# Optimization experiments

Measured on AMD Instinct MI355X. Metric: run time of the kernel, lower is better.

The kernel has to match this reference:

```python
import jax, jax.numpy as jnp
import numpy as np

GROUPS = 32
EPS = 1e-5


def group_norm(x, gamma, beta):
    # x: [B, C, H, W]; normalize over (C//G, H, W) within each of G groups
    B, C, H, W = x.shape
    xg = x.reshape(B, GROUPS, C // GROUPS, H, W)
    mean = xg.mean(axis=(2, 3, 4), keepdims=True)
    var = xg.var(axis=(2, 3, 4), keepdims=True)
    xg = (xg - mean) * jax.lax.rsqrt(var + EPS)
    x = xg.reshape(B, C, H, W)
    return x * gamma[None, :, None, None] + beta[None, :, None, None]


def conv1x1(x, W, b):
    # 1x1 conv == pointwise linear over channels. x: [B,C,H,W], W: [Cout,Cin]
    return jnp.einsum('oc,bchw->bohw', W, x) + b[None, :, None, None]


def setup_inputs() -> dict:
    key = jax.random.key(0)
    ks = jax.random.split(key, 6)
    B, C, H, W = 16, 512, 32, 32
    scale = 1.0 / np.sqrt(C)  # ~kaiming-ish init for 1x1 convs
    return {
        'x': jax.random.normal(ks[0], (B, C, H, W), jnp.float32),
        'gn_gamma': jnp.ones((C,), jnp.float32),
        'gn_beta': jnp.zeros((C,), jnp.float32),
        'Wq': jax.random.normal(ks[1], (C, C), jnp.float32) * scale,
        'bq': jnp.zeros((C,), jnp.float32),
        'Wk': jax.random.normal(ks[2], (C, C), jnp.float32) * scale,
        'bk': jnp.zeros((C,), jnp.float32),
        'Wv': jax.random.normal(ks[3], (C, C), jnp.float32) * scale,
        'bv': jnp.zeros((C,), jnp.float32),
        'Wp': jax.random.normal(ks[4], (C, C), jnp.float32) * scale,
        'bp': jnp.zeros((C,), jnp.float32),
    }


def reference(x, gn_gamma, gn_beta, Wq, bq, Wk, bk, Wv, bv, Wp, bp):
    B, C, H, W = x.shape
    h = group_norm(x, gn_gamma, gn_beta)
    q = conv1x1(h, Wq, bq).reshape(B, C, H * W)  # [B,C,T]
    k = conv1x1(h, Wk, bk).reshape(B, C, H * W)
    v = conv1x1(h, Wv, bv).reshape(B, C, H * W)
    # scores [B, T(query), S(key)] = q^T k, scaled by C^{-1/2}
    w = jnp.einsum('bct,bcs->bts', q, k) * (C ** -0.5)
    w = jax.nn.softmax(w, axis=-1)
    h = jnp.einsum('bts,bcs->bct', w, v).reshape(B, C, H, W)
    h = conv1x1(h, Wp, bp)
    return x + h
```

## Files before the change

### kernel.cpp

```cpp
#include <hip/hip_runtime.h>

typedef unsigned short u16;
typedef __bf16 bf16x8 __attribute__((ext_vector_type(8)));
typedef float f32x16 __attribute__((ext_vector_type(16)));

__device__ __forceinline__ u16 f2bf(float f) {
    unsigned u = __builtin_bit_cast(unsigned, f);
    u += 0x7fffu + ((u >> 16) & 1u);
    return (u16)(u >> 16);
}
__device__ __forceinline__ float bf2f(u16 h) {
    return __builtin_bit_cast(float, (unsigned)h << 16);
}

#define GLDS16(g, l) __builtin_amdgcn_global_load_lds( \
    (const __attribute__((address_space(1))) void*)(g), \
    (__attribute__((address_space(3))) void*)(l), 16, 0, 0)

#define QK_SCALE 0.044194173824159216f

__global__ __launch_bounds__(256) void convert_kernel(
    const float* __restrict__ Wq, const float* __restrict__ Wk,
    const float* __restrict__ Wv, const float* __restrict__ Wp,
    const float* __restrict__ bq, const float* __restrict__ bk,
    const float* __restrict__ bv,
    u16* __restrict__ Wqkv, u16* __restrict__ Wpb, float* __restrict__ bqkv)
{
    int idx = blockIdx.x * 256 + threadIdx.x;
    if (idx < 786432) {
        int which = idx >> 18;
        int off   = idx & 262143;
        if (which == 0)
            Wqkv[idx] = f2bf(Wq[off] * QK_SCALE);
        else
            Wqkv[idx] = f2bf(((which == 1) ? Wk : Wv)[off]);
    } else {
        int off = idx - 786432;
        Wpb[off] = f2bf(Wp[off]);
    }
    if (idx < 1536) {
        float bvv = (idx < 512) ? bq[idx] * QK_SCALE
                  : (idx < 1024) ? bk[idx & 511] : bv[idx & 511];
        bqkv[idx] = bvv;
    }
}

__global__ __launch_bounds__(256) void gn_stats(
    const float* __restrict__ x, float2* __restrict__ stats)
{
    const int g = blockIdx.x, b = blockIdx.y, tid = threadIdx.x;
    const float* xg = x + ((size_t)b * 512 + (size_t)g * 16) * 1024;

    float s = 0.f, s2 = 0.f;
    const float4* x4 = (const float4*)xg;
    #pragma unroll 4
    for (int i = tid; i < 4096; i += 256) {
        float4 v = x4[i];
        s  += v.x + v.y + v.z + v.w;
        s2 += v.x * v.x + v.y * v.y + v.z * v.z + v.w * v.w;
    }
    #pragma unroll
    for (int off = 32; off; off >>= 1) {
        s  += __shfl_down(s, off);
        s2 += __shfl_down(s2, off);
    }
    __shared__ float rs[4], rs2[4];
    const int w = tid >> 6;
    if ((tid & 63) == 0) { rs[w] = s; rs2[w] = s2; }
    __syncthreads();
    if (tid == 0) {
        float S  = rs[0] + rs[1] + rs[2] + rs[3];
        float S2 = rs2[0] + rs2[1] + rs2[2] + rs2[3];
        float mean = S * (1.f / 16384.f);
        float var  = S2 * (1.f / 16384.f) - mean * mean;
        stats[b * 32 + g] = make_float2(mean, rsqrtf(var + 1e-5f));
    }
}

__global__ __launch_bounds__(256) void gn_apply(
    const float* __restrict__ x, const float* __restrict__ gamma,
    const float* __restrict__ beta, const float2* __restrict__ stats,
    u16* __restrict__ ht)
{
    const int tc = blockIdx.x, b = blockIdx.y, tid = threadIdx.x;
    const int t0 = tc * 32;

    __shared__ float2 st[32];
    __shared__ float ga[512], be[512];
    __shared__ __align__(16) u16 tile[512 * 32];

    if (tid < 32) st[tid] = stats[b * 32 + tid];
    for (int c = tid; c < 512; c += 256) { ga[c] = gamma[c]; be[c] = beta[c]; }
    __syncthreads();

    #pragma unroll
    for (int pass = 0; pass < 16; pass++) {
        const int c = pass * 32 + (tid >> 3);
        const int f = tid & 7;
        float4 v = *(const float4*)(x + ((size_t)(b * 512 + c)) * 1024 + t0 + f * 4);
        float2 s = st[c >> 4];
        float sc = s.y * ga[c];
        float sh = be[c] - s.x * sc;
        ushort4 hv = {f2bf(v.x * sc + sh), f2bf(v.y * sc + sh),
                      f2bf(v.z * sc + sh), f2bf(v.w * sc + sh)};
        const int slot = f ^ (c & 7) ^ ((c >> 3) & 7);
        *(ushort4*)(tile + c * 32 + slot * 4) = hv;
    }
    __syncthreads();

    #pragma unroll
    for (int p = 0; p < 8; p++) {
        const int t = p * 4 + (tid >> 6);
        const int l = tid & 63;
        u16 tmp[8];
        #pragma unroll
        for (int e = 0; e < 8; e++) {
            const int c = l * 8 + e;
            const int slot = (t >> 2) ^ (c & 7) ^ ((c >> 3) & 7);
            tmp[e] = tile[c * 32 + slot * 4 + (t & 3)];
        }
        *(uint4*)(ht + ((size_t)b * 1024 + t0 + t) * 512 + l * 8) = *(uint4*)tmp;
    }
}

__global__ __launch_bounds__(256) void softmax_kernel(u16* __restrict__ scores)
{
    const int row  = blockIdx.x * 4 + (threadIdx.x >> 6);
    const int lane = threadIdx.x & 63;
    u16* p = scores + (size_t)row * 1024 + lane * 16;

    uint4 w0 = ((const uint4*)p)[0];
    uint4 w1 = ((const uint4*)p)[1];
    unsigned wd[8] = {w0.x, w0.y, w0.z, w0.w, w1.x, w1.y, w1.z, w1.w};
    float v[16];
    #pragma unroll
    for (int i = 0; i < 8; i++) {
        v[2 * i]     = __builtin_bit_cast(float, wd[i] << 16);
        v[2 * i + 1] = __builtin_bit_cast(float, wd[i] & 0xffff0000u);
    }
    float m = v[0];
    #pragma unroll
    for (int i = 1; i < 16; i++) m = fmaxf(m, v[i]);
    #pragma unroll
    for (int off = 1; off < 64; off <<= 1) m = fmaxf(m, __shfl_xor(m, off));

    float s = 0.f;
    #pragma unroll
    for (int i = 0; i < 16; i++) { v[i] = __expf(v[i] - m); s += v[i]; }
    #pragma unroll
    for (int off = 1; off < 64; off <<= 1) s += __shfl_xor(s, off);
    const float inv = 1.0f / s;

    #pragma unroll
    for (int i = 0; i < 8; i++) {
        unsigned lo = f2bf(v[2 * i] * inv);
        unsigned hi = f2bf(v[2 * i + 1] * inv);
        wd[i] = lo | (hi << 16);
    }
    ((uint4*)p)[0] = make_uint4(wd[0], wd[1], wd[2], wd[3]);
    ((uint4*)p)[1] = make_uint4(wd[4], wd[5], wd[6], wd[7]);
}

template <int MODE>
__global__ __launch_bounds__(256, 4) void gemm_nt(
    const u16* __restrict__ A, const u16* __restrict__ B,
    size_t strideA, size_t strideB, int lda, int ldb, int K,
    u16* __restrict__ o0, u16* __restrict__ o1, u16* __restrict__ o2,
    float* __restrict__ fo, const float* __restrict__ bias,
    const float* __restrict__ xres)
{
    __shared__ __align__(16) u16 sm[16384];
    u16* As = sm;
    u16* Bs = sm + 8192;

    const int tid   = threadIdx.x;
    const int lane  = tid & 63;
    const int wave  = tid >> 6;
    const int wm    = (wave >> 1) * 64;
    const int wn    = (wave & 1) * 64;
    const int l31   = lane & 31;
    const int khalf = lane >> 5;

    const int gx = gridDim.x, gy = gridDim.y;
    int f = blockIdx.x + gx * (blockIdx.y + gy * blockIdx.z);
    const int nwg = gx * gy * (int)gridDim.z;
    f = (f & 7) * (nwg >> 3) + (f >> 3);
    const int bx  = f % gx;
    const int byz = f / gx;
    const int by  = byz % gy;
    const int b   = byz / gy;

    const u16* Ab = A + (size_t)b * strideA + (size_t)by * 128 * lda;
    const u16* Bb = B + (size_t)b * strideB + (size_t)bx * 128 * ldb;

    const int srow = lane >> 3;
    const int sc   = lane & 7;
    const int scg  = sc ^ srow;

    f32x16 acc[2][2] = {};

    for (int k0 = 0; k0 < K; k0 += 64) {
        __syncthreads();
        #pragma unroll
        for (int s = 0; s < 4; s++) {
            const int r = wave * 32 + s * 8 + srow;
            GLDS16(Ab + (size_t)r * lda + k0 + scg * 8, As + r * 64 + sc * 8);
            GLDS16(Bb + (size_t)r * ldb + k0 + scg * 8, Bs + r * 64 + sc * 8);
        }
        __syncthreads();

        #pragma unroll
        for (int ks = 0; ks < 4; ks++) {
            const int cidx = ks * 2 + khalf;
            const int slot = (cidx ^ (lane & 7)) * 8;
            bf16x8 af[2], bfr[2];
            #pragma unroll
            for (int i = 0; i < 2; i++)
                af[i] = *(const bf16x8*)(As + (wm + i * 32 + l31) * 64 + slot);
            #pragma unroll
            for (int j = 0; j < 2; j++)
                bfr[j] = *(const bf16x8*)(Bs + (wn + j * 32 + l31) * 64 + slot);
            #pragma unroll
            for (int i = 0; i < 2; i++)
                #pragma unroll
                for (int j = 0; j < 2; j++)
                    acc[i][j] = __builtin_amdgcn_mfma_f32_32x32x16_bf16(
                        af[i], bfr[j], acc[i][j], 0, 0, 0);
        }
    }

    const int N0 = bx * 128;
    const int M0 = by * 128;

    if (MODE == 0 && N0 < 1024) {
        const int m_base = M0 + wm + 4 * khalf;
        const int n_base = N0 + wn + l31;
        #pragma unroll
        for (int i = 0; i < 2; i++) {
            #pragma unroll
            for (int j = 0; j < 2; j++) {
                const int n  = n_base + j * 32;
                const float bv = bias[n];
                u16* dst = (n < 512) ? o0 : o1;
                const int nn = n & 511;
                #pragma unroll
                for (int g = 0; g < 4; g++) {
                    const int m = m_base + i * 32 + 8 * g;
                    dst[((size_t)b * 1024 + m) * 512 + nn]     = f2bf(acc[i][j][4 * g]     + bv);
                    dst[((size_t)b * 1024 + m + 1) * 512 + nn] = f2bf(acc[i][j][4 * g + 1] + bv);
                    dst[((size_t)b * 1024 + m + 2) * 512 + nn] = f2bf(acc[i][j][4 * g + 2] + bv);
                    dst[((size_t)b * 1024 + m + 3) * 512 + nn] = f2bf(acc[i][j][4 * g + 3] + bv);
                }
            }
        }
    } else if (MODE != 3) {
        __syncthreads();
        #pragma unroll
        for (int i = 0; i < 2; i++) {
            #pragma unroll
            for (int j = 0; j < 2; j++) {
                const int n = wn + j * 32 + l31;
                const float bv = (MODE == 0) ? bias[N0 + n] : 0.f;
                #pragma unroll
                for (int g = 0; g < 4; g++) {
                    const int m = wm + 4 * khalf + i * 32 + 8 * g;
                    ushort4 hv = {f2bf(acc[i][j][4 * g]     + bv),
                                  f2bf(acc[i][j][4 * g + 1] + bv),
                                  f2bf(acc[i][j][4 * g + 2] + bv),
                                  f2bf(acc[i][j][4 * g + 3] + bv)};
                    *(ushort4*)(sm + n * 128 + (((m >> 3) ^ (n & 15)) << 3) + (m & 7)) = hv;
                }
            }
        }
        __syncthreads();
        #pragma unroll
        for (int p = 0; p < 8; p++) {
            const int n  = p * 16 + (tid >> 4);
            const int gi = tid & 15;
            uint4 v = *(const uint4*)(sm + n * 128 + ((gi ^ (n & 15)) << 3));
            u16* dst;
            if (MODE == 0)      dst = o2 + ((size_t)b * 512 + (N0 - 1024 + n)) * 1024 + M0;
            else if (MODE == 1) dst = o0 + ((size_t)b * 1024 + N0 + n) * 1024 + M0;
            else                dst = o0 + ((size_t)b * 1024 + N0 + n) * 512 + M0;
            *(uint4*)(dst + gi * 8) = v;
        }
    } else {
        float* smf = (float*)sm;
        #pragma unroll
        for (int i = 0; i < 2; i++) {
            __syncthreads();
            #pragma unroll
            for (int j = 0; j < 2; j++) {
                const int n = wn + j * 32 + l31;
                #pragma unroll
                for (int g = 0; g < 4; g++) {
                    const int mIdx = 4 * khalf + 8 * g + ((wm >> 6) << 5);
                    float4 v4 = {acc[i][j][4 * g],     acc[i][j][4 * g + 1],
                                 acc[i][j][4 * g + 2], acc[i][j][4 * g + 3]};
                    *(float4*)(smf + n * 64 + (((mIdx >> 2) ^ (n & 15)) << 2)) = v4;
                }
            }
            __syncthreads();
            #pragma unroll
            for (int p = 0; p < 8; p++) {
                const int n  = p * 16 + (tid >> 4);
                const int gi = tid & 15;
                float4 v = *(const float4*)(smf + n * 64 + ((gi ^ (n & 15)) << 2));
                const int m = (gi & 7) * 4 + ((gi >> 3) << 6) + 32 * i;
                const size_t off = ((size_t)b * 512 + N0 + n) * 1024 + M0 + m;
                const float bv = bias[N0 + n];
                const float4 xv = *(const float4*)(xres + off);
                float4 ov = {v.x + bv + xv.x, v.y + bv + xv.y,
                             v.z + bv + xv.z, v.w + bv + xv.w};
                *(float4*)(fo + off) = ov;
            }
        }
    }
}

extern "C" void kernel_launch(void* const* d_in, const int* in_sizes, int n_in,
                              void* d_out, int out_size, void* d_ws, size_t ws_size,
                              hipStream_t stream)
{
    const float* x     = (const float*)d_in[0];
    const float* gamma = (const float*)d_in[1];
    const float* beta  = (const float*)d_in[2];
    const float* Wq    = (const float*)d_in[3];
    const float* bq    = (const float*)d_in[4];
    const float* Wk    = (const float*)d_in[5];
    const float* bk    = (const float*)d_in[6];
    const float* Wv    = (const float*)d_in[7];
    const float* bv    = (const float*)d_in[8];
    const float* Wp    = (const float*)d_in[9];
    const float* bp    = (const float*)d_in[10];

    char* ws = (char*)d_ws;
    u16*   Wqkv   = (u16*)(ws + 0);
    u16*   Wpb    = (u16*)(ws + 1572864);
    float* bqkv   = (float*)(ws + 2097152);
    u16*   ht     = (u16*)(ws + 2105344);
    u16*   kt     = (u16*)(ws + 18882560);
    u16*   vv     = (u16*)(ws + 35659776);
    u16*   scores = (u16*)(ws + 52436992);
    u16*   qt  = (u16*)d_out;
    float2* stats = (float2*)((char*)d_out + 16777216);
    u16*   h2  = ht;
    float* out = (float*)d_out;

    convert_kernel<<<4096, 256, 0, stream>>>(Wq, Wk, Wv, Wp, bq, bk, bv,
                                             Wqkv, Wpb, bqkv);
    gn_stats<<<dim3(32, 16), 256, 0, stream>>>(x, stats);
    gn_apply<<<dim3(32, 16), 256, 0, stream>>>(x, gamma, beta, stats, ht);

    gemm_nt<0><<<dim3(12, 8, 16), 256, 0, stream>>>(
        ht, Wqkv, 524288, 0, 512, 512, 512,
        qt, kt, vv, nullptr, bqkv, nullptr);

    gemm_nt<1><<<dim3(8, 8, 16), 256, 0, stream>>>(
        kt, qt, 524288, 524288, 512, 512, 512,
        scores, nullptr, nullptr, nullptr, nullptr, nullptr);

    softmax_kernel<<<4096, 256, 0, stream>>>(scores);

    gemm_nt<2><<<dim3(8, 4, 16), 256, 0, stream>>>(
        vv, scores, 524288, 1048576, 1024, 1024, 1024,
        h2, nullptr, nullptr, nullptr, nullptr, nullptr);

    gemm_nt<3><<<dim3(4, 8, 16), 256, 0, stream>>>(
        h2, Wpb, 524288, 0, 512, 512, 512,
        nullptr, nullptr, nullptr, out, bp, x);
}
```

Before: 232.2 us.

## Replace GEMM with 256x128 tile, 512-thread, triple-buffered async pipeline

Rewrites the shared GEMM kernel to use 256x128 output tiles with 8 waves and 16x16x32 MFMAs. Global-to-LDS loads are triple-buffered and issued two K-steps ahead with partial vmcnt waits, replacing the synchronous load-then-compute loop. Epilogues are restaged through LDS for coalesced writes, including the Q/K row-major path. It uses much more LDS (144KB) and halves the grid sizes, which lowers occupancy and the number of workgroups.

```diff
diff --git a/kernel.cpp b/kernel.cpp
--- a/kernel.cpp
+++ b/kernel.cpp
@@ -2,15 +2,12 @@
 
 typedef unsigned short u16;
 typedef __bf16 bf16x8 __attribute__((ext_vector_type(8)));
-typedef float f32x16 __attribute__((ext_vector_type(16)));
+typedef float f32x4 __attribute__((ext_vector_type(4)));
 
 __device__ __forceinline__ u16 f2bf(float f) {
     unsigned u = __builtin_bit_cast(unsigned, f);
     u += 0x7fffu + ((u >> 16) & 1u);
     return (u16)(u >> 16);
-}
-__device__ __forceinline__ float bf2f(u16 h) {
-    return __builtin_bit_cast(float, (unsigned)h << 16);
 }
 
 #define GLDS16(g, l) __builtin_amdgcn_global_load_lds( \
@@ -162,24 +159,22 @@
 }
 
 template <int MODE>
-__global__ __launch_bounds__(256, 4) void gemm_nt(
+__global__ __launch_bounds__(512, 2) void gemm_big(
     const u16* __restrict__ A, const u16* __restrict__ B,
     size_t strideA, size_t strideB, int lda, int ldb, int K,
     u16* __restrict__ o0, u16* __restrict__ o1, u16* __restrict__ o2,
     float* __restrict__ fo, const float* __restrict__ bias,
     const float* __restrict__ xres)
 {
-    __shared__ __align__(16) u16 sm[16384];
-    u16* As = sm;
-    u16* Bs = sm + 8192;
-
-    const int tid   = threadIdx.x;
-    const int lane  = tid & 63;
-    const int wave  = tid >> 6;
-    const int wm    = (wave >> 1) * 64;
-    const int wn    = (wave & 1) * 64;
-    const int l31   = lane & 31;
-    const int khalf = lane >> 5;
+    __shared__ __align__(16) u16 smem[73728];
+    u16* As = smem;
+    u16* Bs = smem + 49152;
+
+    const int tid  = threadIdx.x;
+    const int lane = tid & 63;
+    const int wave = tid >> 6;
+    const int wm   = (wave & 3) * 64;
+    const int wn   = (wave >> 2) * 64;
 
     const int gx = gridDim.x, gy = gridDim.y;
     int f = blockIdx.x + gx * (blockIdx.y + gy * blockIdx.z);
@@ -190,130 +185,168 @@
     const int by  = byz % gy;
     const int b   = byz / gy;
 
-    const u16* Ab = A + (size_t)b * strideA + (size_t)by * 128 * lda;
+    const u16* Ab = A + (size_t)b * strideA + (size_t)by * 256 * lda;
     const u16* Bb = B + (size_t)b * strideB + (size_t)bx * 128 * ldb;
 
-    const int srow = lane >> 3;
-    const int sc   = lane & 7;
-    const int scg  = sc ^ srow;
-
-    f32x16 acc[2][2] = {};
-
-    for (int k0 = 0; k0 < K; k0 += 64) {
+    const int srow = tid >> 3;
+    const int sc   = tid & 7;
+    const int scg  = sc ^ (srow & 7);
+
+    const u16* aSrc[4]; int aDst[4];
+    #pragma unroll
+    for (int u = 0; u < 4; u++) {
+        aSrc[u] = Ab + (size_t)(u * 64 + srow) * lda + scg * 8;
+        aDst[u] = (u * 64 + srow) * 64 + sc * 8;
+    }
+    const u16* bSrc[2]; int bDst[2];
+    #pragma unroll
+    for (int u = 0; u < 2; u++) {
+        bSrc[u] = Bb + (size_t)(u * 64 + srow) * ldb + scg * 8;
+        bDst[u] = (u * 64 + srow) * 64 + sc * 8;
+    }
+
+#define STAGEBIG(ko, sb) do { \
+    _Pragma("unroll") \
+    for (int u = 0; u < 4; u++) \
+        GLDS16(aSrc[u] + (ko), As + (sb) * 16384 + aDst[u]); \
+    _Pragma("unroll") \
+    for (int u = 0; u < 2; u++) \
+        GLDS16(bSrc[u] + (ko), Bs + (sb) * 8192 + bDst[u]); \
+} while (0)
+
+    const int l15 = lane & 15, lh = lane >> 4, rx = lane & 7;
+    int aOff[4][2], bOff[4][2];
+    #pragma unroll
+    for (int i = 0; i < 4; i++)
+        #pragma unroll
+        for (int ks = 0; ks < 2; ks++) {
+            const int slot = ((ks << 2) + lh) ^ rx;
+            aOff[i][ks] = (wm + i * 16 + l15) * 64 + slot * 8;
+            bOff[i][ks] = (wn + i * 16 + l15) * 64 + slot * 8;
+        }
+
+    f32x4 acc[4][4] = {};
+    const int NT = K >> 6;
+
+    STAGEBIG(0, 0);
+    STAGEBIG(64, 1);
+
+    int cbuf = 0, sbuf = 2;
+    for (int t = 0; t < NT; ++t) {
+        if (t == NT - 1) asm volatile("s_waitcnt vmcnt(0)" ::: "memory");
+        else             asm volatile("s_waitcnt vmcnt(6)" ::: "memory");
+        __builtin_amdgcn_s_barrier();
+        __builtin_amdgcn_sched_barrier(0);
+
+        if (t + 2 < NT) STAGEBIG((t + 2) * 64, sbuf);
+        __builtin_amdgcn_sched_barrier(0);
+
+        const u16* Ac = As + cbuf * 16384;
+        const u16* Bc = Bs + cbuf * 8192;
+        bf16x8 af[4][2], bf[4][2];
+        #pragma unroll
+        for (int i = 0; i < 4; i++)
+            #pragma unroll
+            for (int ks = 0; ks < 2; ks++) {
+                af[i][ks] = *(const bf16x8*)(Ac + aOff[i][ks]);
+                bf[i][ks] = *(const bf16x8*)(Bc + bOff[i][ks]);
+            }
+
+        __builtin_amdgcn_s_setprio(1);
+        #pragma unroll
+        for (int ks = 0; ks < 2; ks++)
+            #pragma unroll
+            for (int mi = 0; mi < 4; mi++)
+                #pragma unroll
+                for (int nj = 0; nj < 4; nj++)
+                    acc[mi][nj] = __builtin_amdgcn_mfma_f32_16x16x32_bf16(
+                        af[mi][ks], bf[nj][ks], acc[mi][nj], 0, 0, 0);
+        __builtin_amdgcn_s_setprio(0);
+
+        cbuf = (cbuf == 2) ? 0 : cbuf + 1;
+        sbuf = (sbuf == 2) ? 0 : sbuf + 1;
+    }
+#undef STAGEBIG
+
+    const int N0 = bx * 128;
+    const int M0 = by * 256;
+
+    __syncthreads();
+
+    if (MODE != 3) {
+        #pragma unroll
+        for (int mi = 0; mi < 4; mi++) {
+            const int mq = wm + mi * 16 + lh * 4;
+            #pragma unroll
+            for (int nj = 0; nj < 4; nj++) {
+                const int n = wn + nj * 16 + l15;
+                float bv = 0.f;
+                if (MODE == 0) bv = bias[N0 + n];
+                ushort4 hv = {f2bf(acc[mi][nj][0] + bv), f2bf(acc[mi][nj][1] + bv),
+                              f2bf(acc[mi][nj][2] + bv), f2bf(acc[mi][nj][3] + bv)};
+                *(ushort4*)((char*)smem + n * 512 +
+                            ((((mq >> 3) ^ (n & 31))) << 4) + ((mq >> 2) & 1) * 8) = hv;
+            }
+        }
         __syncthreads();
-        #pragma unroll
-        for (int s = 0; s < 4; s++) {
-            const int r = wave * 32 + s * 8 + srow;
-            GLDS16(Ab + (size_t)r * lda + k0 + scg * 8, As + r * 64 + sc * 8);
-            GLDS16(Bb + (size_t)r * ldb + k0 + scg * 8, Bs + r * 64 + sc * 8);
+
+        if (MODE == 0 && N0 < 1024) {
+            #pragma unroll
+            for (int p = 0; p < 8; p++) {
+                const int m  = p * 32 + (tid >> 4);
+                const int ci = tid & 15;
+                u16 tmp[8];
+                #pragma unroll
+                for (int e = 0; e < 8; e++) {
+                    const int n = ci * 8 + e;
+                    tmp[e] = *(const u16*)((char*)smem + n * 512 +
+                             (((m >> 3) ^ (n & 31)) << 4) + (m & 7) * 2);
+                }
+                u16* dst = (N0 < 512) ? o0 : o1;
+                const int nn = (N0 & 511) + ci * 8;
+                *(uint4*)(dst + ((size_t)b * 1024 + M0 + m) * 512 + nn) = *(uint4*)tmp;
+            }
+        } else {
+            #pragma unroll
+            for (int p = 0; p < 8; p++) {
+                const int n  = p * 16 + (tid >> 5);
+                const int gi = tid & 31;
+                uint4 v4 = *(const uint4*)((char*)smem + n * 512 +
+                                           ((gi ^ (n & 31)) << 4));
+                u16* dst;
+                if (MODE == 0)      dst = o2 + ((size_t)b * 512 + (N0 - 1024) + n) * 1024 + M0;
+                else if (MODE == 1) dst = o0 + ((size_t)b * 1024 + N0 + n) * 1024 + M0;
+                else                dst = o0 + ((size_t)b * 1024 + N0 + n) * 512 + M0;
+                *(uint4*)(dst + gi * 8) = v4;
+            }
+        }
+    } else {
+        float* smf = (float*)smem;
+        #pragma unroll
+        for (int mi = 0; mi < 4; mi++) {
+            const int mq = wm + mi * 16 + lh * 4;
+            #pragma unroll
+            for (int nj = 0; nj < 4; nj++) {
+                const int n = wn + nj * 16 + l15;
+                float4 v4 = {acc[mi][nj][0], acc[mi][nj][1],
+                             acc[mi][nj][2], acc[mi][nj][3]};
+                *(float4*)((char*)smf + n * 1024 +
+                           (((mq >> 2) ^ (n & 63)) << 4)) = v4;
+            }
         }
         __syncthreads();
-
-        #pragma unroll
-        for (int ks = 0; ks < 4; ks++) {
-            const int cidx = ks * 2 + khalf;
-            const int slot = (cidx ^ (lane & 7)) * 8;
-            bf16x8 af[2], bfr[2];
-            #pragma unroll
-            for (int i = 0; i < 2; i++)
-                af[i] = *(const bf16x8*)(As + (wm + i * 32 + l31) * 64 + slot);
-            #pragma unroll
-            for (int j = 0; j < 2; j++)
-                bfr[j] = *(const bf16x8*)(Bs + (wn + j * 32 + l31) * 64 + slot);
-            #pragma unroll
-            for (int i = 0; i < 2; i++)
-                #pragma unroll
-                for (int j = 0; j < 2; j++)
-                    acc[i][j] = __builtin_amdgcn_mfma_f32_32x32x16_bf16(
-                        af[i], bfr[j], acc[i][j], 0, 0, 0);
-        }
-    }
-
-    const int N0 = bx * 128;
-    const int M0 = by * 128;
-
-    if (MODE == 0 && N0 < 1024) {
-        const int m_base = M0 + wm + 4 * khalf;
-        const int n_base = N0 + wn + l31;
-        #pragma unroll
-        for (int i = 0; i < 2; i++) {
-            #pragma unroll
-            for (int j = 0; j < 2; j++) {
-                const int n  = n_base + j * 32;
-                const float bv = bias[n];
-                u16* dst = (n < 512) ? o0 : o1;
-                const int nn = n & 511;
-                #pragma unroll
-                for (int g = 0; g < 4; g++) {
-                    const int m = m_base + i * 32 + 8 * g;
-                    dst[((size_t)b * 1024 + m) * 512 + nn]     = f2bf(acc[i][j][4 * g]     + bv);
-                    dst[((size_t)b * 1024 + m + 1) * 512 + nn] = f2bf(acc[i][j][4 * g + 1] + bv);
-                    dst[((size_t)b * 1024 + m + 2) * 512 + nn] = f2bf(acc[i][j][4 * g + 2] + bv);
-                    dst[((size_t)b * 1024 + m + 3) * 512 + nn] = f2bf(acc[i][j][4 * g + 3] + bv);
-                }
-            }
-        }
-    } else if (MODE != 3) {
-        __syncthreads();
-        #pragma unroll
-        for (int i = 0; i < 2; i++) {
-            #pragma unroll
-            for (int j = 0; j < 2; j++) {
-                const int n = wn + j * 32 + l31;
-                const float bv = (MODE == 0) ? bias[N0 + n] : 0.f;
-                #pragma unroll
-                for (int g = 0; g < 4; g++) {
-                    const int m = wm + 4 * khalf + i * 32 + 8 * g;
-                    ushort4 hv = {f2bf(acc[i][j][4 * g]     + bv),
-                                  f2bf(acc[i][j][4 * g + 1] + bv),
-                                  f2bf(acc[i][j][4 * g + 2] + bv),
-                                  f2bf(acc[i][j][4 * g + 3] + bv)};
-                    *(ushort4*)(sm + n * 128 + (((m >> 3) ^ (n & 15)) << 3) + (m & 7)) = hv;
-                }
-            }
-        }
-        __syncthreads();
-        #pragma unroll
-        for (int p = 0; p < 8; p++) {
-            const int n  = p * 16 + (tid >> 4);
-            const int gi = tid & 15;
-            uint4 v = *(const uint4*)(sm + n * 128 + ((gi ^ (n & 15)) << 3));
-            u16* dst;
-            if (MODE == 0)      dst = o2 + ((size_t)b * 512 + (N0 - 1024 + n)) * 1024 + M0;
-            else if (MODE == 1) dst = o0 + ((size_t)b * 1024 + N0 + n) * 1024 + M0;
-            else                dst = o0 + ((size_t)b * 1024 + N0 + n) * 512 + M0;
-            *(uint4*)(dst + gi * 8) = v;
-        }
-    } else {
-        float* smf = (float*)sm;
-        #pragma unroll
-        for (int i = 0; i < 2; i++) {
-            __syncthreads();
-            #pragma unroll
-            for (int j = 0; j < 2; j++) {
-                const int n = wn + j * 32 + l31;
-                #pragma unroll
-                for (int g = 0; g < 4; g++) {
-                    const int mIdx = 4 * khalf + 8 * g + ((wm >> 6) << 5);
-                    float4 v4 = {acc[i][j][4 * g],     acc[i][j][4 * g + 1],
-                                 acc[i][j][4 * g + 2], acc[i][j][4 * g + 3]};
-                    *(float4*)(smf + n * 64 + (((mIdx >> 2) ^ (n & 15)) << 2)) = v4;
-                }
-            }
-            __syncthreads();
-            #pragma unroll
-            for (int p = 0; p < 8; p++) {
-                const int n  = p * 16 + (tid >> 4);
-                const int gi = tid & 15;
-                float4 v = *(const float4*)(smf + n * 64 + ((gi ^ (n & 15)) << 2));
-                const int m = (gi & 7) * 4 + ((gi >> 3) << 6) + 32 * i;
-                const size_t off = ((size_t)b * 512 + N0 + n) * 1024 + M0 + m;
-                const float bv = bias[N0 + n];
-                const float4 xv = *(const float4*)(xres + off);
-                float4 ov = {v.x + bv + xv.x, v.y + bv + xv.y,
-                             v.z + bv + xv.z, v.w + bv + xv.w};
-                *(float4*)(fo + off) = ov;
-            }
+        #pragma unroll
+        for (int p = 0; p < 16; p++) {
+            const int n  = p * 8 + (tid >> 6);
+            const int gi = tid & 63;
+            float4 v4 = *(const float4*)((char*)smf + n * 1024 +
+                                         ((gi ^ (n & 63)) << 4));
+            const size_t off = ((size_t)b * 512 + N0 + n) * 1024 + M0 + gi * 4;
+            const float bv = bias[N0 + n];
+            const float4 xv = *(const float4*)(xres + off);
+            float4 ov = {v4.x + bv + xv.x, v4.y + bv + xv.y,
+                         v4.z + bv + xv.z, v4.w + bv + xv.w};
+            *(float4*)(fo + off) = ov;
         }
     }
 }
@@ -352,21 +385,21 @@
     gn_stats<<<dim3(32, 16), 256, 0, stream>>>(x, stats);
     gn_apply<<<dim3(32, 16), 256, 0, stream>>>(x, gamma, beta, stats, ht);
 
-    gemm_nt<0><<<dim3(12, 8, 16), 256, 0, stream>>>(
+    gemm_big<0><<<dim3(12, 4, 16), 512, 0, stream>>>(
         ht, Wqkv, 524288, 0, 512, 512, 512,
         qt, kt, vv, nullptr, bqkv, nullptr);
 
-    gemm_nt<1><<<dim3(8, 8, 16), 256, 0, stream>>>(
+    gemm_big<1><<<dim3(8, 4, 16), 512, 0, stream>>>(
         kt, qt, 524288, 524288, 512, 512, 512,
         scores, nullptr, nullptr, nullptr, nullptr, nullptr);
 
     softmax_kernel<<<4096, 256, 0, stream>>>(scores);
 
-    gemm_nt<2><<<dim3(8, 4, 16), 256, 0, stream>>>(
+    gemm_big<2><<<dim3(8, 2, 16), 512, 0, stream>>>(
         vv, scores, 524288, 1048576, 1024, 1024, 1024,
         h2, nullptr, nullptr, nullptr, nullptr, nullptr);
 
-    gemm_nt<3><<<dim3(4, 8, 16), 256, 0, stream>>>(
+    gemm_big<3><<<dim3(4, 4, 16), 512, 0, stream>>>(
         h2, Wpb, 524288, 0, 512, 512, 512,
         nullptr, nullptr, nullptr, out, bp, x);
 }
```

Result: slower. 241.2 us (+3.9%).

## Fuse softmax into QK^T epilogue and PV normalization via row-sum atomics

Applied to the files above, without the earlier changes.

Removes the separate softmax kernel. The QK^T GEMM epilogue now writes exp(scores) without subtracting the row max and atomically adds per-row sums into a buffer. The PV GEMM then scales by the reciprocal of that sum. This avoids one full read-write pass over the bf16 score matrix. The cost is atomics and a loss of numerical safety, since exp without max subtraction can overflow for large logits.

```diff
diff --git a/kernel.cpp b/kernel.cpp
--- a/kernel.cpp
+++ b/kernel.cpp
@@ -24,7 +24,8 @@
     const float* __restrict__ Wv, const float* __restrict__ Wp,
     const float* __restrict__ bq, const float* __restrict__ bk,
     const float* __restrict__ bv,
-    u16* __restrict__ Wqkv, u16* __restrict__ Wpb, float* __restrict__ bqkv)
+    u16* __restrict__ Wqkv, u16* __restrict__ Wpb, float* __restrict__ bqkv,
+    float* __restrict__ rsum)
 {
     int idx = blockIdx.x * 256 + threadIdx.x;
     if (idx < 786432) {
@@ -43,6 +44,7 @@
                   : (idx < 1024) ? bk[idx & 511] : bv[idx & 511];
         bqkv[idx] = bvv;
     }
+    if (idx < 16384) rsum[idx] = 0.f;
 }
 
 __global__ __launch_bounds__(256) void gn_stats(
@@ -123,44 +125,6 @@
     }
 }
 
-__global__ __launch_bounds__(256) void softmax_kernel(u16* __restrict__ scores)
-{
-    const int row  = blockIdx.x * 4 + (threadIdx.x >> 6);
-    const int lane = threadIdx.x & 63;
-    u16* p = scores + (size_t)row * 1024 + lane * 16;
-
-    uint4 w0 = ((const uint4*)p)[0];
-    uint4 w1 = ((const uint4*)p)[1];
-    unsigned wd[8] = {w0.x, w0.y, w0.z, w0.w, w1.x, w1.y, w1.z, w1.w};
-    float v[16];
-    #pragma unroll
-    for (int i = 0; i < 8; i++) {
-        v[2 * i]     = __builtin_bit_cast(float, wd[i] << 16);
-        v[2 * i + 1] = __builtin_bit_cast(float, wd[i] & 0xffff0000u);
-    }
-    float m = v[0];
-    #pragma unroll
-    for (int i = 1; i < 16; i++) m = fmaxf(m, v[i]);
-    #pragma unroll
-    for (int off = 1; off < 64; off <<= 1) m = fmaxf(m, __shfl_xor(m, off));
-
-    float s = 0.f;
-    #pragma unroll
-    for (int i = 0; i < 16; i++) { v[i] = __expf(v[i] - m); s += v[i]; }
-    #pragma unroll
-    for (int off = 1; off < 64; off <<= 1) s += __shfl_xor(s, off);
-    const float inv = 1.0f / s;
-
-    #pragma unroll
-    for (int i = 0; i < 8; i++) {
-        unsigned lo = f2bf(v[2 * i] * inv);
-        unsigned hi = f2bf(v[2 * i + 1] * inv);
-        wd[i] = lo | (hi << 16);
-    }
-    ((uint4*)p)[0] = make_uint4(wd[0], wd[1], wd[2], wd[3]);
-    ((uint4*)p)[1] = make_uint4(wd[4], wd[5], wd[6], wd[7]);
-}
-
 template <int MODE>
 __global__ __launch_bounds__(256, 4) void gemm_nt(
     const u16* __restrict__ A, const u16* __restrict__ B,
@@ -255,6 +219,12 @@
         }
     } else if (MODE != 3) {
         __syncthreads();
+        float rinv_[2];
+        if (MODE == 2) {
+            #pragma unroll
+            for (int j = 0; j < 2; j++)
+                rinv_[j] = 1.0f / xres[(size_t)b * 1024 + N0 + wn + j * 32 + l31];
+        }
         #pragma unroll
         for (int i = 0; i < 2; i++) {
             #pragma unroll
@@ -264,10 +234,18 @@
                 #pragma unroll
                 for (int g = 0; g < 4; g++) {
                     const int m = wm + 4 * khalf + i * 32 + 8 * g;
-                    ushort4 hv = {f2bf(acc[i][j][4 * g]     + bv),
-                                  f2bf(acc[i][j][4 * g + 1] + bv),
-                                  f2bf(acc[i][j][4 * g + 2] + bv),
-                                  f2bf(acc[i][j][4 * g + 3] + bv)};
+                    float a0 = acc[i][j][4 * g],     a1 = acc[i][j][4 * g + 1];
+                    float a2 = acc[i][j][4 * g + 2], a3 = acc[i][j][4 * g + 3];
+                    if (MODE == 0) { a0 += bv; a1 += bv; a2 += bv; a3 += bv; }
+                    if (MODE == 1) {
+                        a0 = __expf(a0); a1 = __expf(a1);
+                        a2 = __expf(a2); a3 = __expf(a3);
+                    }
+                    if (MODE == 2) {
+                        a0 *= rinv_[j]; a1 *= rinv_[j];
+                        a2 *= rinv_[j]; a3 *= rinv_[j];
+                    }
+                    ushort4 hv = {f2bf(a0), f2bf(a1), f2bf(a2), f2bf(a3)};
                     *(ushort4*)(sm + n * 128 + (((m >> 3) ^ (n & 15)) << 3) + (m & 7)) = hv;
                 }
             }
@@ -283,6 +261,19 @@
             else if (MODE == 1) dst = o0 + ((size_t)b * 1024 + N0 + n) * 1024 + M0;
             else                dst = o0 + ((size_t)b * 1024 + N0 + n) * 512 + M0;
             *(uint4*)(dst + gi * 8) = v;
+            if (MODE == 1) {
+                unsigned wd_[4] = {v.x, v.y, v.z, v.w};
+                float rsm = 0.f;
+                #pragma unroll
+                for (int q = 0; q < 4; q++)
+                    rsm += __builtin_bit_cast(float, wd_[q] << 16)
+                         + __builtin_bit_cast(float, wd_[q] & 0xffff0000u);
+                #pragma unroll
+                for (int off = 1; off < 16; off <<= 1)
+                    rsm += __shfl_xor(rsm, off);
+                if (gi == 0)
+                    atomicAdd(fo + ((size_t)b * 1024 + N0 + n), rsm);
+            }
         }
     } else {
         float* smf = (float*)sm;
@@ -344,11 +335,12 @@
     u16*   scores = (u16*)(ws + 52436992);
     u16*   qt  = (u16*)d_out;
     float2* stats = (float2*)((char*)d_out + 16777216);
+    float* rsum   = (float*)((char*)d_out + 16781312);
     u16*   h2  = ht;
     float* out = (float*)d_out;
 
     convert_kernel<<<4096, 256, 0, stream>>>(Wq, Wk, Wv, Wp, bq, bk, bv,
-                                             Wqkv, Wpb, bqkv);
+                                             Wqkv, Wpb, bqkv, rsum);
     gn_stats<<<dim3(32, 16), 256, 0, stream>>>(x, stats);
     gn_apply<<<dim3(32, 16), 256, 0, stream>>>(x, gamma, beta, stats, ht);
 
@@ -358,13 +350,11 @@
 
     gemm_nt<1><<<dim3(8, 8, 16), 256, 0, stream>>>(
         kt, qt, 524288, 524288, 512, 512, 512,
-        scores, nullptr, nullptr, nullptr, nullptr, nullptr);
-
-    softmax_kernel<<<4096, 256, 0, stream>>>(scores);
+        scores, nullptr, nullptr, rsum, nullptr, nullptr);
 
     gemm_nt<2><<<dim3(8, 4, 16), 256, 0, stream>>>(
         vv, scores, 524288, 1048576, 1024, 1024, 1024,
-        h2, nullptr, nullptr, nullptr, nullptr, nullptr);
+        h2, nullptr, nullptr, nullptr, nullptr, rsum);
 
     gemm_nt<3><<<dim3(4, 8, 16), 256, 0, stream>>>(
         h2, Wpb, 524288, 0, 512, 512, 512,
```

Result: faster. 217.8 us (-6.2%).
